# Performance work log

Measured on AMD Instinct MI355X. Metric: run time of the kernel, lower is better.

## Reference

```python
import jax, jax.numpy as jnp
import numpy as np

B, L, EMB = 256, 200, 128   # batch, low_capsule_num, emb_dim
HCN, HD = 1000, 64          # h_caps_num = poi_num//20, h_caps_dim
POI = 20000
EPS = 1e-8


def squash(s):
    # standard capsule squash along last dim
    sq = jnp.sum(s * s, axis=-1, keepdims=True)
    return (sq / (1.0 + sq)) * s / jnp.sqrt(sq + EPS)


def setup_inputs() -> dict:
    key = jax.random.key(0)
    ks = jax.random.split(key, 5)
    return {
        "u": jax.random.normal(ks[0], (B, L, EMB), jnp.float32),
        "l_map_h": jax.random.normal(ks[1], (EMB, HD), jnp.float32),
        "route_weights": jax.random.normal(ks[2], (1, HCN, L), jnp.float32),
        "w_dim": jax.random.normal(ks[3], (1, HD), jnp.float32) * 0.1,
        "b_dim": jnp.zeros((1,), jnp.float32),
        "w_part": jax.random.normal(ks[4], (POI, HCN), jnp.float32) * 0.03,
        "b_part": jnp.zeros((POI,), jnp.float32),
        "rn": 3,
    }


def reference(u, l_map_h, route_weights, w_dim, b_dim, w_part, b_part, rn):
    # u: [B, L, EMB] -> u_map: [B, L, HD]
    u_map = jnp.matmul(u, l_map_h)
    b = route_weights  # [1, HCN, L], non-trainable in the original
    v = None
    for _ in range(rn):
        c = jax.nn.softmax(b, axis=-1)            # [1, HCN, L]
        s = jnp.matmul(c, u_map)                  # broadcast -> [B, HCN, HD]
        v = squash(s)                             # [B, HCN, HD]
        # torch: sum over batch of v @ u_map^T, keepdim; .data update (detached)
        u_v = jnp.einsum('bhd,bld->hl', v, u_map)[None]  # [1, HCN, L]
        b = b + jax.lax.stop_gradient(u_v)
    # dim_linear_1 (Linear(HD,1)) then squeeze; dropout is identity (eval)
    h = jnp.squeeze(jnp.matmul(v, w_dim.T) + b_dim, axis=-1)  # [B, HCN]
    out = jnp.matmul(h, w_part.T) + b_part                     # [B, POI]
    return out
```

## Files before the change

### kernel.cpp

```cpp
#include <hip/hip_runtime.h>

#define B_    256
#define L_    200
#define EMB_  128
#define HD_   64
#define HCN_  1000
#define POI_  20000
#define EPS_  1e-8f
#define CP    224
#define UNR   208
#define NSLAB 64
#define SROW  1024
#define SPL   208

#define CSC   16384.0f
#define USC   256.0f
#define VSC   1024.0f
#define AUSC  1024.0f
#define LUSC  1024.0f
#define SV_DESC (1.0f / (CSC * USC))
#define UV_DESC (1.0f / (VSC * USC))
#define UM_DESC (1.0f / (AUSC * LUSC))

typedef _Float16 half8 __attribute__((ext_vector_type(8)));
typedef __bf16  bf16x8 __attribute__((ext_vector_type(8)));
typedef float   f32x4  __attribute__((ext_vector_type(4)));
typedef float   f32x16 __attribute__((ext_vector_type(16)));

__device__ __forceinline__ unsigned short f2bf(float f) {
  union { float f; unsigned int u; } v; v.f = f;
  unsigned int r = (v.u + 0x7FFFu + ((v.u >> 16) & 1u)) >> 16;
  return (unsigned short)r;
}
__device__ __forceinline__ void split2h(float x, _Float16& s1, _Float16& s2) {
  s1 = (_Float16)x;
  s2 = (_Float16)(x - (float)s1);
}

#define THREEPASS(acc, A1f, A2f, B1f, B2f)                                 \
  acc = __builtin_amdgcn_mfma_f32_16x16x32_f16(A2f, B1f, acc, 0, 0, 0);    \
  acc = __builtin_amdgcn_mfma_f32_16x16x32_f16(A1f, B2f, acc, 0, 0, 0);    \
  acc = __builtin_amdgcn_mfma_f32_16x16x32_f16(A1f, B1f, acc, 0, 0, 0);

__global__ __launch_bounds__(256, 2) void k_umap(const float* __restrict__ u,
                                                 const float* __restrict__ lmap,
                                                 float* __restrict__ umap) {
  __shared__ __align__(16) _Float16 lmT[2][64][136];
  __shared__ __align__(16) _Float16 uA[4][2][16][136];
  const int tid = threadIdx.x;
  for (int i = tid; i < 128 * 64; i += 256) {
    int k = i >> 6, d = i & 63;
    _Float16 s1, s2;
    split2h(lmap[i] * LUSC, s1, s2);
    lmT[0][d][k] = s1;
    lmT[1][d][k] = s2;
  }
  __syncthreads();

  const int wave = tid >> 6, lane = tid & 63;
  const int l15 = lane & 15, oc = lane >> 4;

  for (int t = 0; t < 4; ++t) {
    const int row0 = (blockIdx.x * 16 + wave * 4 + t) * 16;
    {
      const int r_ = lane >> 2, seg = lane & 3;
      const float* src = u + (size_t)(row0 + r_) * EMB_ + seg * 32;
#pragma unroll
      for (int j = 0; j < 8; ++j) {
        float4 v = *(const float4*)(src + j * 4);
        _Float16 t1[4], t2[4];
        split2h(v.x * AUSC, t1[0], t2[0]);
        split2h(v.y * AUSC, t1[1], t2[1]);
        split2h(v.z * AUSC, t1[2], t2[2]);
        split2h(v.w * AUSC, t1[3], t2[3]);
        const int kb = seg * 32 + j * 4;
        *(uint2*)&uA[wave][0][r_][kb] = *(uint2*)t1;
        *(uint2*)&uA[wave][1][r_][kb] = *(uint2*)t2;
      }
    }
    f32x4 acc[4] = {};
#pragma unroll
    for (int ck = 0; ck < 4; ++ck) {
      const half8 a1 = *(const half8*)&uA[wave][0][l15][ck * 32 + oc * 8];
      const half8 a2 = *(const half8*)&uA[wave][1][l15][ck * 32 + oc * 8];
#pragma unroll
      for (int nt = 0; nt < 4; ++nt) {
        const half8 b1 = *(const half8*)&lmT[0][nt * 16 + l15][ck * 32 + oc * 8];
        const half8 b2 = *(const half8*)&lmT[1][nt * 16 + l15][ck * 32 + oc * 8];
        THREEPASS(acc[nt], a1, a2, b1, b2);
      }
    }
#pragma unroll
    for (int nt = 0; nt < 4; ++nt)
#pragma unroll
      for (int r = 0; r < 4; ++r)
        umap[(size_t)(row0 + oc * 4 + r) * HD_ + nt * 16 + l15] = acc[nt][r] * UM_DESC;
  }
}

__global__ __launch_bounds__(256) void k_prep2(const float* __restrict__ umap,
    _Float16* __restrict__ un1, _Float16* __restrict__ un2,
    _Float16* __restrict__ ut1, _Float16* __restrict__ ut2) {
  __shared__ __align__(16) float us[CP][68];
  const int b = blockIdx.x;
  const float* ub = umap + (size_t)b * L_ * HD_;
  for (int i = threadIdx.x; i < CP * HD_; i += 256) {
    int l = i >> 6, d = i & 63;
    us[l][d] = (l < L_) ? ub[l * HD_ + d] * USC : 0.f;
  }
  __syncthreads();
  for (int s = threadIdx.x; s < UNR * 8; s += 256) {
    int row = s >> 3, oct = s & 7;
    _Float16 t1[8], t2[8];
#pragma unroll
    for (int j = 0; j < 8; ++j) split2h(us[row][oct * 8 + j], t1[j], t2[j]);
    size_t dst = ((size_t)b * UNR + row) * HD_ + oct * 8;
    *(uint4*)&un1[dst] = *(uint4*)t1;
    *(uint4*)&un2[dst] = *(uint4*)t2;
  }
  for (int s = threadIdx.x; s < HD_ * 28; s += 256) {
    int d = s / 28, lo8 = s % 28;
    _Float16 t1[8], t2[8];
#pragma unroll
    for (int j = 0; j < 8; ++j) split2h(us[lo8 * 8 + j][d], t1[j], t2[j]);
    size_t dst = ((size_t)b * HD_ + d) * CP + lo8 * 8;
    *(uint4*)&ut1[dst] = *(uint4*)t1;
    *(uint4*)&ut2[dst] = *(uint4*)t2;
  }
}

template<int SUM>
__global__ __launch_bounds__(256) void k_softmax2(float* __restrict__ bl,
    const float* __restrict__ part,
    _Float16* __restrict__ c1, _Float16* __restrict__ c2) {
  const int wave = threadIdx.x >> 6, lane = threadIdx.x & 63;
  const int row = blockIdx.x * 4 + wave;
  const size_t rb = (size_t)row * CP;
  if (row >= HCN_) {
    c1[rb + lane] = (_Float16)0.f;       c2[rb + lane] = (_Float16)0.f;
    c1[rb + lane + 64] = (_Float16)0.f;  c2[rb + lane + 64] = (_Float16)0.f;
    c1[rb + lane + 128] = (_Float16)0.f; c2[rb + lane + 128] = (_Float16)0.f;
    if (lane < 32) { c1[rb + 192 + lane] = (_Float16)0.f; c2[rb + 192 + lane] = (_Float16)0.f; }
    return;
  }
  float* br = bl + (size_t)row * L_;
  float x0 = br[lane];
  float x1 = br[lane + 64];
  float x2 = br[lane + 128];
  float x3 = (lane < 8) ? br[lane + 192] : -3.0e38f;
  if (SUM) {
#pragma unroll 8
    for (int s = 0; s < NSLAB; ++s) {
      const float* p = part + ((size_t)s * SROW + row) * SPL;
      x0 += __builtin_nontemporal_load(p + lane);
      x1 += __builtin_nontemporal_load(p + lane + 64);
      x2 += __builtin_nontemporal_load(p + lane + 128);
      if (lane < 8) x3 += __builtin_nontemporal_load(p + lane + 192);
    }
    br[lane] = x0; br[lane + 64] = x1; br[lane + 128] = x2;
    if (lane < 8) br[lane + 192] = x3;
  }
  float m = fmaxf(fmaxf(x0, x1), fmaxf(x2, x3));
#pragma unroll
  for (int off = 32; off; off >>= 1) m = fmaxf(m, __shfl_xor(m, off));
  float e0 = expf(x0 - m), e1 = expf(x1 - m), e2 = expf(x2 - m);
  float e3 = (lane < 8) ? expf(x3 - m) : 0.f;
  float ssum = e0 + e1 + e2 + e3;
#pragma unroll
  for (int off = 32; off; off >>= 1) ssum += __shfl_xor(ssum, off);
  float inv = CSC / ssum;
  _Float16 s1, s2;
  split2h(e0 * inv, s1, s2); c1[rb + lane] = s1;       c2[rb + lane] = s2;
  split2h(e1 * inv, s1, s2); c1[rb + lane + 64] = s1;  c2[rb + lane + 64] = s2;
  split2h(e2 * inv, s1, s2); c1[rb + lane + 128] = s1; c2[rb + lane + 128] = s2;
  if (lane < 8) {
    split2h(e3 * inv, s1, s2); c1[rb + 192 + lane] = s1; c2[rb + 192 + lane] = s2;
  } else if (lane < 32) {
    c1[rb + 192 + lane] = (_Float16)0.f; c2[rb + 192 + lane] = (_Float16)0.f;
  }
}

template<int UV, int HOUT>
__global__ __launch_bounds__(256, 4) void k_iter(
    const _Float16* __restrict__ c1p, const _Float16* __restrict__ c2p,
    const _Float16* __restrict__ un1, const _Float16* __restrict__ un2,
    const _Float16* __restrict__ ut1, const _Float16* __restrict__ ut2,
    const float* __restrict__ wdim, const float* __restrict__ bdim,
    float* __restrict__ part, unsigned short* __restrict__ hb) {
  __shared__ __align__(16) _Float16 smem[10240];
  __shared__ __align__(16) _Float16 v_sm[UV ? (2 * 64 * 72) : 2];
  typedef _Float16 (*UTarr)[2][64][40];
  typedef _Float16 (*UNarr)[112][40];
  typedef _Float16 (*VSarr)[64][72];
  UTarr UT = reinterpret_cast<UTarr>(smem);
  UNarr UN = reinterpret_cast<UNarr>(smem);
  VSarr VS = reinterpret_cast<VSarr>(v_sm);

  const int id = blockIdx.x;
  const int xcd = id & 7;
  const int ht  = (id >> 3) & 15;
  const int bgH = id >> 7;
  const int bg  = xcd + (bgH << 3);
  const int h0 = ht * 64;
  const int b0 = bg * 4;
  const int tid = threadIdx.x;
  const int wave = tid >> 6, lane = tid & 63;
  const int l15 = lane & 15, oc = lane >> 4;
  const int rowA = h0 + wave * 16 + l15;
  const int rowC = h0 + wave * 16 + oc * 4;

#define STAGE_UT(cck, bf) {                                                    \
    const int d_ = tid >> 2, q_ = tid & 3;                                     \
    const size_t so_ = ((size_t)b * HD_ + d_) * CP + (cck) * 32 + q_ * 8;      \
    *(uint4*)&UT[bf][0][d_][q_ * 8] = *(const uint4*)&ut1[so_];                \
    *(uint4*)&UT[bf][1][d_][q_ * 8] = *(const uint4*)&ut2[so_];                \
  }

#define STAGE_UN2(half_, g_, nrows_) {                                        \
    _Pragma("unroll")                                                          \
    for (int j_ = 0; j_ < 2; ++j_) {                                           \
      int t_ = tid + 256 * j_;                                                 \
      if (t_ < (nrows_) * 4) {                                                 \
        int row_ = t_ >> 2, q_ = t_ & 3;                                       \
        const size_t so_ = ((size_t)b * UNR + (g_) * 112 + row_) * HD_         \
                           + (half_) * 32 + q_ * 8;                            \
        *(uint4*)&UN[0][row_][q_ * 8] = *(const uint4*)&un1[so_];              \
        *(uint4*)&UN[1][row_][q_ * 8] = *(const uint4*)&un2[so_];              \
      } } }

  half8 a_f[7][2];
#pragma unroll
  for (int ck = 0; ck < 7; ++ck) {
    const size_t off = (size_t)rowA * CP + ck * 32 + oc * 8;
    a_f[ck][0] = *(const half8*)&c1p[off];
    a_f[ck][1] = *(const half8*)&c2p[off];
  }

  f32x4 acc_uv[13];
  if (UV) {
#pragma unroll
    for (int nt = 0; nt < 13; ++nt) acc_uv[nt] = (f32x4){0.f, 0.f, 0.f, 0.f};
  }
  float wd[4] = {0.f, 0.f, 0.f, 0.f};
  float bd = 0.f;
  if (HOUT) {
#pragma unroll
    for (int nt = 0; nt < 4; ++nt) wd[nt] = wdim[nt * 16 + l15];
    bd = bdim[0];
  }

  for (int bi = 0; bi < 4; ++bi) {
    const int b = b0 + bi;
    f32x4 acc_s[4];
#pragma unroll
    for (int nt = 0; nt < 4; ++nt) acc_s[nt] = (f32x4){0.f, 0.f, 0.f, 0.f};
    STAGE_UT(0, 0);
    __syncthreads();
#pragma unroll
    for (int ck = 0; ck < 7; ++ck) {
      if (ck < 6) STAGE_UT(ck + 1, (ck + 1) & 1);
      const int cb = ck & 1;
#pragma unroll
      for (int nt = 0; nt < 4; ++nt) {
        const half8 b1 = *(const half8*)&UT[cb][0][nt * 16 + l15][oc * 8];
        const half8 b2 = *(const half8*)&UT[cb][1][nt * 16 + l15][oc * 8];
        THREEPASS(acc_s[nt], a_f[ck][0], a_f[ck][1], b1, b2);
      }
      __syncthreads();
    }
    float xdesc[4][4];
#pragma unroll
    for (int nt = 0; nt < 4; ++nt)
#pragma unroll
      for (int r = 0; r < 4; ++r) xdesc[nt][r] = acc_s[nt][r] * SV_DESC;
    float gg[4], hq[4];
#pragma unroll
    for (int r = 0; r < 4; ++r) {
      float sq = 0.f, hpp = 0.f;
#pragma unroll
      for (int nt = 0; nt < 4; ++nt) {
        float x = xdesc[nt][r];
        sq += x * x;
        if (HOUT) hpp += x * wd[nt];
      }
#pragma unroll
      for (int off = 8; off; off >>= 1) {
        sq += __shfl_xor(sq, off);
        if (HOUT) hpp += __shfl_xor(hpp, off);
      }
      gg[r] = sq / ((1.f + sq) * sqrtf(sq + EPS_));
      if (HOUT) hq[r] = gg[r] * hpp + bd;
    }
    if (HOUT && l15 == 0) {
      ushort4 hv4;
      if (rowC < HCN_) {
        hv4.x = f2bf(hq[0]); hv4.y = f2bf(hq[1]);
        hv4.z = f2bf(hq[2]); hv4.w = f2bf(hq[3]);
      } else {
        hv4.x = hv4.y = hv4.z = hv4.w = 0;
      }
      *(ushort4*)&hb[(size_t)b * 1024 + rowC] = hv4;
    }
    if (UV) {
#pragma unroll
      for (int nt = 0; nt < 4; ++nt)
#pragma unroll
        for (int r = 0; r < 4; ++r) {
          _Float16 s1, s2;
          split2h(VSC * gg[r] * xdesc[nt][r], s1, s2);
          const int vr = wave * 16 + oc * 4 + r, vc = nt * 16 + l15;
          VS[0][vr][vc] = s1; VS[1][vr][vc] = s2;
        }
      __syncthreads();
#pragma unroll
      for (int half = 0; half < 2; ++half) {
        const int vo = half * 32 + oc * 8;
        const half8 av1 = *(const half8*)&VS[0][wave * 16 + l15][vo];
        const half8 av2 = *(const half8*)&VS[1][wave * 16 + l15][vo];
#pragma unroll
        for (int g = 0; g < 2; ++g) {
          STAGE_UN2(half, g, (g ? 96 : 112));
          __syncthreads();
          if (g == 0) {
#pragma unroll
            for (int nt = 0; nt < 7; ++nt) {
              const half8 b1 = *(const half8*)&UN[0][nt * 16 + l15][oc * 8];
              const half8 b2 = *(const half8*)&UN[1][nt * 16 + l15][oc * 8];
              THREEPASS(acc_uv[nt], av1, av2, b1, b2);
            }
          } else {
#pragma unroll
            for (int nt = 7; nt < 13; ++nt) {
              const half8 b1 = *(const half8*)&UN[0][(nt - 7) * 16 + l15][oc * 8];
              const half8 b2 = *(const half8*)&UN[1][(nt - 7) * 16 + l15][oc * 8];
              THREEPASS(acc_uv[nt], av1, av2, b1, b2);
            }
          }
          __syncthreads();
        }
      }
    }
  }
  if (UV) {
    float* pp = part + (size_t)bg * SROW * SPL;
#pragma unroll
    for (int r = 0; r < 4; ++r) {
      float* rowp = pp + (size_t)(rowC + r) * SPL + l15;
#pragma unroll
      for (int nt = 0; nt < 13; ++nt)
        __builtin_nontemporal_store(acc_uv[nt][r] * UV_DESC, rowp + nt * 16);
    }
  }
#undef STAGE_UT
#undef STAGE_UN2
}

#define KPAD 1024
#define LPITCH 72
__global__ __launch_bounds__(512) void k_out_mfma(const unsigned short* __restrict__ hb,
                                                  const float* __restrict__ wpart,
                                                  const float* __restrict__ bpart,
                                                  float* __restrict__ out) {
  __shared__ __align__(16) unsigned short w_lds[128 * LPITCH];
  __shared__ __align__(16) unsigned short h_lds[128 * LPITCH];
  const int p0 = blockIdx.x * 128;
  const int b0 = blockIdx.y * 128;
  const int t = threadIdx.x;
  const int wave = t >> 6, lane = t & 63;
  const int nt = wave & 3, mh = wave >> 2;
  const int l31 = lane & 31, lhi = lane >> 5;

  f32x16 acc0 = {};
  f32x16 acc1 = {};

  const int wrow = t >> 2;
  const int wq0  = (t & 3) * 4;
  int prow = p0 + wrow; if (prow > POI_ - 1) prow = POI_ - 1;
  const float* wrp = wpart + (size_t)prow * HCN_;

  for (int ch = 0; ch < 16; ++ch) {
    const int k0 = ch * 64;
    __syncthreads();
#pragma unroll
    for (int qq = 0; qq < 4; ++qq) {
      const int q = wq0 + qq;
      float4 wv;
      if (k0 + q * 4 + 3 < HCN_) {
        wv = *(const float4*)(wrp + k0 + q * 4);
      } else {
        float x0 = (k0 + q * 4 + 0 < HCN_) ? wrp[k0 + q * 4 + 0] : 0.f;
        float x1 = (k0 + q * 4 + 1 < HCN_) ? wrp[k0 + q * 4 + 1] : 0.f;
        float x2 = (k0 + q * 4 + 2 < HCN_) ? wrp[k0 + q * 4 + 2] : 0.f;
        float x3 = (k0 + q * 4 + 3 < HCN_) ? wrp[k0 + q * 4 + 3] : 0.f;
        wv = make_float4(x0, x1, x2, x3);
      }
      ushort4 bv;
      bv.x = f2bf(wv.x); bv.y = f2bf(wv.y); bv.z = f2bf(wv.z); bv.w = f2bf(wv.w);
      *(ushort4*)&w_lds[wrow * LPITCH + q * 4] = bv;
    }
#pragma unroll
    for (int n = 0; n < 2; ++n) {
      const int u = t + n * 512;
      const int hrow = u >> 3, hc = u & 7;
      const uint4 hv = *(const uint4*)(hb + (size_t)(b0 + hrow) * KPAD + k0 + hc * 8);
      *(uint4*)&h_lds[hrow * LPITCH + hc * 8] = hv;
    }
    __syncthreads();
#pragma unroll
    for (int ks = 0; ks < 4; ++ks) {
      const int kc = ks * 16 + lhi * 8;
      bf16x8 bfr = *(const bf16x8*)&w_lds[(nt * 32 + l31) * LPITCH + kc];
      bf16x8 a0  = *(const bf16x8*)&h_lds[(mh * 64 + 0 * 32 + l31) * LPITCH + kc];
      bf16x8 a1  = *(const bf16x8*)&h_lds[(mh * 64 + 1 * 32 + l31) * LPITCH + kc];
      acc0 = __builtin_amdgcn_mfma_f32_32x32x16_bf16(a0, bfr, acc0, 0, 0, 0);
      acc1 = __builtin_amdgcn_mfma_f32_32x32x16_bf16(a1, bfr, acc1, 0, 0, 0);
    }
  }

  const int p = p0 + nt * 32 + l31;
  const bool pok = (p < POI_);
  const float bp = pok ? bpart[p] : 0.f;
#pragma unroll
  for (int m = 0; m < 2; ++m) {
    const f32x16& a = m ? acc1 : acc0;
#pragma unroll
    for (int r = 0; r < 16; ++r) {
      const int brow = b0 + mh * 64 + m * 32 + (r & 3) + 8 * (r >> 2) + 4 * lhi;
      if (pok) out[(size_t)brow * POI_ + p] = a[r] + bp;
    }
  }
}

extern "C" void kernel_launch(void* const* d_in, const int* in_sizes, int n_in,
                              void* d_out, int out_size, void* d_ws, size_t ws_size,
                              hipStream_t stream) {
  const float* u     = (const float*)d_in[0];
  const float* lmap  = (const float*)d_in[1];
  const float* rw    = (const float*)d_in[2];
  const float* wdim  = (const float*)d_in[3];
  const float* bdim  = (const float*)d_in[4];
  const float* wpart = (const float*)d_in[5];
  const float* bpart = (const float*)d_in[6];
  float* out = (float*)d_out;

  char* W = (char*)d_ws;
  float* bl        = (float*)W;      W += 802816;
  _Float16* c1     = (_Float16*)W;   W += 458752;
  _Float16* c2     = (_Float16*)W;   W += 458752;
  _Float16* un1    = (_Float16*)W;   W += 6815744;
  _Float16* un2    = (_Float16*)W;   W += 6815744;
  _Float16* ut1    = (_Float16*)W;   W += 7340032;
  _Float16* ut2    = (_Float16*)W;   W += 7340032;
  unsigned short* h_bf16 = (unsigned short*)W; W += 524288;
  float* part      = (float*)W;      W += (size_t)NSLAB * SROW * SPL * 4;
  float* umap      = part;

  hipMemcpyAsync(bl, rw, (size_t)HCN_ * L_ * sizeof(float),
                 hipMemcpyDeviceToDevice, stream);
  k_umap<<<200, 256, 0, stream>>>(u, lmap, umap);
  k_prep2<<<256, 256, 0, stream>>>(umap, un1, un2, ut1, ut2);

  k_softmax2<0><<<256, 256, 0, stream>>>(bl, part, c1, c2);
  k_iter<1, 0><<<1024, 256, 0, stream>>>(c1, c2, un1, un2, ut1, ut2,
                                         wdim, bdim, part, h_bf16);
  k_softmax2<1><<<256, 256, 0, stream>>>(bl, part, c1, c2);
  k_iter<1, 0><<<1024, 256, 0, stream>>>(c1, c2, un1, un2, ut1, ut2,
                                         wdim, bdim, part, h_bf16);
  k_softmax2<1><<<256, 256, 0, stream>>>(bl, part, c1, c2);
  k_iter<0, 1><<<1024, 256, 0, stream>>>(c1, c2, un1, un2, ut1, ut2,
                                         wdim, bdim, part, h_bf16);

  k_out_mfma<<<dim3(157, 2), 512, 0, stream>>>(h_bf16, wpart, bpart, out);
}
```

Before: 380.5 us.

## Double k_iter block to 512 threads with 8 batches and split work across wave halves

k_iter now runs 512-thread blocks. Each block handles 8 batches instead of 4, which halves the number of partial-sum slabs and the grid size. The two wave halves split the HD dimension for the s computation and combine squared norms through shared memory. They also split the L columns for the u_v accumulation, and the full 208-row u_map slice is staged at once instead of in two chunks. This aims to cut partial-slab write and reduce traffic and barrier count, at the cost of extra LDS use, a cross-wave reduction sync, and possibly lower occupancy.

```diff
diff --git a/kernel.cpp b/kernel.cpp
--- a/kernel.cpp
+++ b/kernel.cpp
@@ -9,7 +9,7 @@
 #define EPS_  1e-8f
 #define CP    224
 #define UNR   208
-#define NSLAB 64
+#define NSLAB 32
 #define SROW  1024
 #define SPL   208
 
@@ -181,16 +181,18 @@
 }
 
 template<int UV, int HOUT>
-__global__ __launch_bounds__(256, 4) void k_iter(
+__global__ __launch_bounds__(512, 4) void k_iter(
     const _Float16* __restrict__ c1p, const _Float16* __restrict__ c2p,
     const _Float16* __restrict__ un1, const _Float16* __restrict__ un2,
     const _Float16* __restrict__ ut1, const _Float16* __restrict__ ut2,
     const float* __restrict__ wdim, const float* __restrict__ bdim,
     float* __restrict__ part, unsigned short* __restrict__ hb) {
-  __shared__ __align__(16) _Float16 smem[10240];
+  __shared__ __align__(16) _Float16 smem[16640];
   __shared__ __align__(16) _Float16 v_sm[UV ? (2 * 64 * 72) : 2];
+  __shared__ __align__(16) float sqx[2][64];
+  __shared__ __align__(16) float hpx[2][64];
   typedef _Float16 (*UTarr)[2][64][40];
-  typedef _Float16 (*UNarr)[112][40];
+  typedef _Float16 (*UNarr)[208][40];
   typedef _Float16 (*VSarr)[64][72];
   UTarr UT = reinterpret_cast<UTarr>(smem);
   UNarr UN = reinterpret_cast<UNarr>(smem);
@@ -202,28 +204,29 @@
   const int bgH = id >> 7;
   const int bg  = xcd + (bgH << 3);
   const int h0 = ht * 64;
-  const int b0 = bg * 4;
+  const int b0 = bg * 8;
   const int tid = threadIdx.x;
   const int wave = tid >> 6, lane = tid & 63;
+  const int hsub = wave & 3, ksub = wave >> 2;
   const int l15 = lane & 15, oc = lane >> 4;
-  const int rowA = h0 + wave * 16 + l15;
-  const int rowC = h0 + wave * 16 + oc * 4;
+  const int rowA = h0 + hsub * 16 + l15;
+  const int rowL = hsub * 16 + oc * 4;
+  const int rowC = h0 + rowL;
 
 #define STAGE_UT(cck, bf) {                                                    \
-    const int d_ = tid >> 2, q_ = tid & 3;                                     \
-    const size_t so_ = ((size_t)b * HD_ + d_) * CP + (cck) * 32 + q_ * 8;      \
-    *(uint4*)&UT[bf][0][d_][q_ * 8] = *(const uint4*)&ut1[so_];                \
-    *(uint4*)&UT[bf][1][d_][q_ * 8] = *(const uint4*)&ut2[so_];                \
-  }
-
-#define STAGE_UN2(half_, g_, nrows_) {                                        \
+    const int sp_ = tid >> 8, d_ = (tid >> 2) & 63, q_ = tid & 3;              \
+    const _Float16* s_ = sp_ ? ut2 : ut1;                                      \
+    *(uint4*)&UT[bf][sp_][d_][q_ * 8] =                                        \
+      *(const uint4*)&s_[((size_t)b * HD_ + d_) * CP + (cck) * 32 + q_ * 8];   \
+  }
+
+#define STAGE_UN(half_) {                                                      \
     _Pragma("unroll")                                                          \
     for (int j_ = 0; j_ < 2; ++j_) {                                           \
-      int t_ = tid + 256 * j_;                                                 \
-      if (t_ < (nrows_) * 4) {                                                 \
+      int t_ = tid + 512 * j_;                                                 \
+      if (t_ < 832) {                                                          \
         int row_ = t_ >> 2, q_ = t_ & 3;                                       \
-        const size_t so_ = ((size_t)b * UNR + (g_) * 112 + row_) * HD_         \
-                           + (half_) * 32 + q_ * 8;                            \
+        const size_t so_ = ((size_t)b * UNR + row_) * HD_ + (half_) * 32 + q_ * 8; \
         *(uint4*)&UN[0][row_][q_ * 8] = *(const uint4*)&un1[so_];              \
         *(uint4*)&UN[1][row_][q_ * 8] = *(const uint4*)&un2[so_];              \
       } } }
@@ -236,24 +239,24 @@
     a_f[ck][1] = *(const half8*)&c2p[off];
   }
 
-  f32x4 acc_uv[13];
+  f32x4 acc_uv[7];
   if (UV) {
 #pragma unroll
-    for (int nt = 0; nt < 13; ++nt) acc_uv[nt] = (f32x4){0.f, 0.f, 0.f, 0.f};
-  }
-  float wd[4] = {0.f, 0.f, 0.f, 0.f};
+    for (int nt = 0; nt < 7; ++nt) acc_uv[nt] = (f32x4){0.f, 0.f, 0.f, 0.f};
+  }
+  float wd[2] = {0.f, 0.f};
   float bd = 0.f;
   if (HOUT) {
 #pragma unroll
-    for (int nt = 0; nt < 4; ++nt) wd[nt] = wdim[nt * 16 + l15];
+    for (int j = 0; j < 2; ++j) wd[j] = wdim[(ksub * 2 + j) * 16 + l15];
     bd = bdim[0];
   }
 
-  for (int bi = 0; bi < 4; ++bi) {
+  for (int bi = 0; bi < 8; ++bi) {
     const int b = b0 + bi;
-    f32x4 acc_s[4];
-#pragma unroll
-    for (int nt = 0; nt < 4; ++nt) acc_s[nt] = (f32x4){0.f, 0.f, 0.f, 0.f};
+    f32x4 acc_s[2];
+#pragma unroll
+    for (int j = 0; j < 2; ++j) acc_s[j] = (f32x4){0.f, 0.f, 0.f, 0.f};
     STAGE_UT(0, 0);
     __syncthreads();
 #pragma unroll
@@ -261,37 +264,49 @@
       if (ck < 6) STAGE_UT(ck + 1, (ck + 1) & 1);
       const int cb = ck & 1;
 #pragma unroll
-      for (int nt = 0; nt < 4; ++nt) {
-        const half8 b1 = *(const half8*)&UT[cb][0][nt * 16 + l15][oc * 8];
-        const half8 b2 = *(const half8*)&UT[cb][1][nt * 16 + l15][oc * 8];
-        THREEPASS(acc_s[nt], a_f[ck][0], a_f[ck][1], b1, b2);
+      for (int j = 0; j < 2; ++j) {
+        const half8 b1 = *(const half8*)&UT[cb][0][(ksub * 2 + j) * 16 + l15][oc * 8];
+        const half8 b2 = *(const half8*)&UT[cb][1][(ksub * 2 + j) * 16 + l15][oc * 8];
+        THREEPASS(acc_s[j], a_f[ck][0], a_f[ck][1], b1, b2);
       }
       __syncthreads();
     }
-    float xdesc[4][4];
-#pragma unroll
-    for (int nt = 0; nt < 4; ++nt)
-#pragma unroll
-      for (int r = 0; r < 4; ++r) xdesc[nt][r] = acc_s[nt][r] * SV_DESC;
-    float gg[4], hq[4];
+    float xd[2][4];
+#pragma unroll
+    for (int j = 0; j < 2; ++j)
+#pragma unroll
+      for (int r = 0; r < 4; ++r) xd[j][r] = acc_s[j][r] * SV_DESC;
+    float sqp[4], hpp[4];
 #pragma unroll
     for (int r = 0; r < 4; ++r) {
-      float sq = 0.f, hpp = 0.f;
-#pragma unroll
-      for (int nt = 0; nt < 4; ++nt) {
-        float x = xdesc[nt][r];
-        sq += x * x;
-        if (HOUT) hpp += x * wd[nt];
-      }
+      float sq = xd[0][r] * xd[0][r] + xd[1][r] * xd[1][r];
+      float hp = 0.f;
+      if (HOUT) hp = xd[0][r] * wd[0] + xd[1][r] * wd[1];
 #pragma unroll
       for (int off = 8; off; off >>= 1) {
         sq += __shfl_xor(sq, off);
-        if (HOUT) hpp += __shfl_xor(hpp, off);
-      }
-      gg[r] = sq / ((1.f + sq) * sqrtf(sq + EPS_));
-      if (HOUT) hq[r] = gg[r] * hpp + bd;
-    }
-    if (HOUT && l15 == 0) {
+        if (HOUT) hp += __shfl_xor(hp, off);
+      }
+      sqp[r] = sq;
+      hpp[r] = hp;
+    }
+    if (l15 == 0) {
+#pragma unroll
+      for (int r = 0; r < 4; ++r) {
+        sqx[ksub][rowL + r] = sqp[r];
+        if (HOUT) hpx[ksub][rowL + r] = hpp[r];
+      }
+    }
+    if (UV) STAGE_UN(0);
+    __syncthreads();
+    float gg[4], hq[4];
+#pragma unroll
+    for (int r = 0; r < 4; ++r) {
+      float st = sqp[r] + sqx[1 - ksub][rowL + r];
+      gg[r] = st / ((1.f + st) * sqrtf(st + EPS_));
+      if (HOUT) hq[r] = gg[r] * (hpp[r] + hpx[1 - ksub][rowL + r]) + bd;
+    }
+    if (HOUT && ksub == 0 && l15 == 0) {
       ushort4 hv4;
       if (rowC < HCN_) {
         hv4.x = f2bf(hq[0]); hv4.y = f2bf(hq[1]);
@@ -303,56 +318,50 @@
     }
     if (UV) {
 #pragma unroll
-      for (int nt = 0; nt < 4; ++nt)
+      for (int j = 0; j < 2; ++j)
 #pragma unroll
         for (int r = 0; r < 4; ++r) {
           _Float16 s1, s2;
-          split2h(VSC * gg[r] * xdesc[nt][r], s1, s2);
-          const int vr = wave * 16 + oc * 4 + r, vc = nt * 16 + l15;
+          split2h(VSC * gg[r] * xd[j][r], s1, s2);
+          const int vr = rowL + r, vc = (ksub * 2 + j) * 16 + l15;
           VS[0][vr][vc] = s1; VS[1][vr][vc] = s2;
         }
       __syncthreads();
 #pragma unroll
       for (int half = 0; half < 2; ++half) {
-        const int vo = half * 32 + oc * 8;
-        const half8 av1 = *(const half8*)&VS[0][wave * 16 + l15][vo];
-        const half8 av2 = *(const half8*)&VS[1][wave * 16 + l15][vo];
-#pragma unroll
-        for (int g = 0; g < 2; ++g) {
-          STAGE_UN2(half, g, (g ? 96 : 112));
+        if (half == 1) {
           __syncthreads();
-          if (g == 0) {
-#pragma unroll
-            for (int nt = 0; nt < 7; ++nt) {
-              const half8 b1 = *(const half8*)&UN[0][nt * 16 + l15][oc * 8];
-              const half8 b2 = *(const half8*)&UN[1][nt * 16 + l15][oc * 8];
-              THREEPASS(acc_uv[nt], av1, av2, b1, b2);
-            }
-          } else {
-#pragma unroll
-            for (int nt = 7; nt < 13; ++nt) {
-              const half8 b1 = *(const half8*)&UN[0][(nt - 7) * 16 + l15][oc * 8];
-              const half8 b2 = *(const half8*)&UN[1][(nt - 7) * 16 + l15][oc * 8];
-              THREEPASS(acc_uv[nt], av1, av2, b1, b2);
-            }
-          }
+          STAGE_UN(1);
           __syncthreads();
         }
-      }
+        const int vo = half * 32 + oc * 8;
+        const half8 av1 = *(const half8*)&VS[0][hsub * 16 + l15][vo];
+        const half8 av2 = *(const half8*)&VS[1][hsub * 16 + l15][vo];
+#pragma unroll
+        for (int nt = 0; nt < 7; ++nt) {
+          int urow = (nt + ksub * 7) * 16 + l15;
+          if (urow > 207) urow = 207;
+          const half8 b1 = *(const half8*)&UN[0][urow][oc * 8];
+          const half8 b2 = *(const half8*)&UN[1][urow][oc * 8];
+          THREEPASS(acc_uv[nt], av1, av2, b1, b2);
+        }
+      }
+      __syncthreads();
     }
   }
   if (UV) {
     float* pp = part + (size_t)bg * SROW * SPL;
 #pragma unroll
     for (int r = 0; r < 4; ++r) {
-      float* rowp = pp + (size_t)(rowC + r) * SPL + l15;
-#pragma unroll
-      for (int nt = 0; nt < 13; ++nt)
-        __builtin_nontemporal_store(acc_uv[nt][r] * UV_DESC, rowp + nt * 16);
+      float* rowp = pp + (size_t)(rowC + r) * SPL + ksub * 112 + l15;
+#pragma unroll
+      for (int nt = 0; nt < 7; ++nt)
+        if (nt + ksub * 7 <= 12)
+          __builtin_nontemporal_store(acc_uv[nt][r] * UV_DESC, rowp + nt * 16);
     }
   }
 #undef STAGE_UT
-#undef STAGE_UN2
+#undef STAGE_UN
 }
 
 #define KPAD 1024
@@ -461,14 +470,14 @@
   k_prep2<<<256, 256, 0, stream>>>(umap, un1, un2, ut1, ut2);
 
   k_softmax2<0><<<256, 256, 0, stream>>>(bl, part, c1, c2);
-  k_iter<1, 0><<<1024, 256, 0, stream>>>(c1, c2, un1, un2, ut1, ut2,
-                                         wdim, bdim, part, h_bf16);
+  k_iter<1, 0><<<512, 512, 0, stream>>>(c1, c2, un1, un2, ut1, ut2,
+                                        wdim, bdim, part, h_bf16);
   k_softmax2<1><<<256, 256, 0, stream>>>(bl, part, c1, c2);
-  k_iter<1, 0><<<1024, 256, 0, stream>>>(c1, c2, un1, un2, ut1, ut2,
-                                         wdim, bdim, part, h_bf16);
+  k_iter<1, 0><<<512, 512, 0, stream>>>(c1, c2, un1, un2, ut1, ut2,
+                                        wdim, bdim, part, h_bf16);
   k_softmax2<1><<<256, 256, 0, stream>>>(bl, part, c1, c2);
-  k_iter<0, 1><<<1024, 256, 0, stream>>>(c1, c2, un1, un2, ut1, ut2,
-                                         wdim, bdim, part, h_bf16);
+  k_iter<0, 1><<<512, 512, 0, stream>>>(c1, c2, un1, un2, ut1, ut2,
+                                        wdim, bdim, part, h_bf16);
 
   k_out_mfma<<<dim3(157, 2), 512, 0, stream>>>(h_bf16, wpart, bpart, out);
 }
```

Measured after the change: 366.0 us. 3.8% less time.

## Double k_iter block tile to 128 capsules and widen LDS staging chunks

Applied to the files above, without the earlier changes.

Each k_iter block now handles 128 high capsules with 8 waves (512 threads) instead of 64 with 4 waves. This halves the grid and the number of times each u_map slab is staged per batch row. The UT staging chunks grow from 32 to 64 columns, and the UN stage loads all 208 rows at once, which cuts the number of syncthreads rounds. In exchange the kernel uses more LDS per block and fewer blocks, so occupancy and latency hiding may drop.

```diff
diff --git a/kernel.cpp b/kernel.cpp
--- a/kernel.cpp
+++ b/kernel.cpp
@@ -181,49 +181,61 @@
 }
 
 template<int UV, int HOUT>
-__global__ __launch_bounds__(256, 4) void k_iter(
+__global__ __launch_bounds__(512, 2) void k_iter(
     const _Float16* __restrict__ c1p, const _Float16* __restrict__ c2p,
     const _Float16* __restrict__ un1, const _Float16* __restrict__ un2,
     const _Float16* __restrict__ ut1, const _Float16* __restrict__ ut2,
     const float* __restrict__ wdim, const float* __restrict__ bdim,
     float* __restrict__ part, unsigned short* __restrict__ hb) {
-  __shared__ __align__(16) _Float16 smem[10240];
-  __shared__ __align__(16) _Float16 v_sm[UV ? (2 * 64 * 72) : 2];
-  typedef _Float16 (*UTarr)[2][64][40];
-  typedef _Float16 (*UNarr)[112][40];
-  typedef _Float16 (*VSarr)[64][72];
+  __shared__ __align__(16) _Float16 smem[18432];
+  __shared__ __align__(16) _Float16 v_sm[UV ? (2 * 128 * 72) : 2];
+  typedef _Float16 (*UTarr)[2][64][72];
+  typedef _Float16 (*UNarr)[208][40];
+  typedef _Float16 (*VSarr)[128][72];
   UTarr UT = reinterpret_cast<UTarr>(smem);
   UNarr UN = reinterpret_cast<UNarr>(smem);
   VSarr VS = reinterpret_cast<VSarr>(v_sm);
 
   const int id = blockIdx.x;
   const int xcd = id & 7;
-  const int ht  = (id >> 3) & 15;
-  const int bgH = id >> 7;
+  const int ht  = (id >> 3) & 7;
+  const int bgH = id >> 6;
   const int bg  = xcd + (bgH << 3);
-  const int h0 = ht * 64;
+  const int h0 = ht * 128;
   const int b0 = bg * 4;
   const int tid = threadIdx.x;
   const int wave = tid >> 6, lane = tid & 63;
   const int l15 = lane & 15, oc = lane >> 4;
   const int rowA = h0 + wave * 16 + l15;
-  const int rowC = h0 + wave * 16 + oc * 4;
-
-#define STAGE_UT(cck, bf) {                                                    \
-    const int d_ = tid >> 2, q_ = tid & 3;                                     \
-    const size_t so_ = ((size_t)b * HD_ + d_) * CP + (cck) * 32 + q_ * 8;      \
-    *(uint4*)&UT[bf][0][d_][q_ * 8] = *(const uint4*)&ut1[so_];                \
-    *(uint4*)&UT[bf][1][d_][q_ * 8] = *(const uint4*)&ut2[so_];                \
-  }
-
-#define STAGE_UN2(half_, g_, nrows_) {                                        \
+  const int rowL = wave * 16 + oc * 4;
+  const int rowC = h0 + rowL;
+
+#define STAGE_UT64(cck, bf) {                                                  \
     _Pragma("unroll")                                                          \
     for (int j_ = 0; j_ < 2; ++j_) {                                           \
-      int t_ = tid + 256 * j_;                                                 \
-      if (t_ < (nrows_) * 4) {                                                 \
+      int s_ = tid + 512 * j_;                                                 \
+      int sp_ = s_ >> 9, rem_ = s_ & 511;                                      \
+      int d_ = rem_ >> 3, q_ = rem_ & 7;                                       \
+      const _Float16* src_ = sp_ ? ut2 : ut1;                                  \
+      *(uint4*)&UT[bf][sp_][d_][q_ * 8] =                                      \
+        *(const uint4*)&src_[((size_t)b * HD_ + d_) * CP + (cck) * 64 + q_ * 8]; \
+    } }
+
+#define STAGE_UT32(bf) {                                                       \
+    int sp_ = tid >> 8, rem_ = tid & 255;                                      \
+    int d_ = rem_ >> 2, q_ = rem_ & 3;                                         \
+    const _Float16* src_ = sp_ ? ut2 : ut1;                                    \
+    *(uint4*)&UT[bf][sp_][d_][q_ * 8] =                                        \
+      *(const uint4*)&src_[((size_t)b * HD_ + d_) * CP + 192 + q_ * 8];        \
+  }
+
+#define STAGE_UN(half_) {                                                      \
+    _Pragma("unroll")                                                          \
+    for (int j_ = 0; j_ < 2; ++j_) {                                           \
+      int t_ = tid + 512 * j_;                                                 \
+      if (t_ < 832) {                                                          \
         int row_ = t_ >> 2, q_ = t_ & 3;                                       \
-        const size_t so_ = ((size_t)b * UNR + (g_) * 112 + row_) * HD_         \
-                           + (half_) * 32 + q_ * 8;                            \
+        const size_t so_ = ((size_t)b * UNR + row_) * HD_ + (half_) * 32 + q_ * 8; \
         *(uint4*)&UN[0][row_][q_ * 8] = *(const uint4*)&un1[so_];              \
         *(uint4*)&UN[1][row_][q_ * 8] = *(const uint4*)&un2[so_];              \
       } } }
@@ -254,19 +266,29 @@
     f32x4 acc_s[4];
 #pragma unroll
     for (int nt = 0; nt < 4; ++nt) acc_s[nt] = (f32x4){0.f, 0.f, 0.f, 0.f};
-    STAGE_UT(0, 0);
+    STAGE_UT64(0, 0);
     __syncthreads();
 #pragma unroll
-    for (int ck = 0; ck < 7; ++ck) {
-      if (ck < 6) STAGE_UT(ck + 1, (ck + 1) & 1);
+    for (int ck = 0; ck < 3; ++ck) {
+      if (ck < 2) STAGE_UT64(ck + 1, (ck + 1) & 1)
+      else        STAGE_UT32(1)
       const int cb = ck & 1;
 #pragma unroll
       for (int nt = 0; nt < 4; ++nt) {
-        const half8 b1 = *(const half8*)&UT[cb][0][nt * 16 + l15][oc * 8];
-        const half8 b2 = *(const half8*)&UT[cb][1][nt * 16 + l15][oc * 8];
-        THREEPASS(acc_s[nt], a_f[ck][0], a_f[ck][1], b1, b2);
-      }
-      __syncthreads();
+#pragma unroll
+        for (int sub = 0; sub < 2; ++sub) {
+          const half8 b1 = *(const half8*)&UT[cb][0][nt * 16 + l15][sub * 32 + oc * 8];
+          const half8 b2 = *(const half8*)&UT[cb][1][nt * 16 + l15][sub * 32 + oc * 8];
+          THREEPASS(acc_s[nt], a_f[ck * 2 + sub][0], a_f[ck * 2 + sub][1], b1, b2);
+        }
+      }
+      __syncthreads();
+    }
+#pragma unroll
+    for (int nt = 0; nt < 4; ++nt) {
+      const half8 b1 = *(const half8*)&UT[1][0][nt * 16 + l15][oc * 8];
+      const half8 b2 = *(const half8*)&UT[1][1][nt * 16 + l15][oc * 8];
+      THREEPASS(acc_s[nt], a_f[6][0], a_f[6][1], b1, b2);
     }
     float xdesc[4][4];
 #pragma unroll
@@ -308,37 +330,38 @@
         for (int r = 0; r < 4; ++r) {
           _Float16 s1, s2;
           split2h(VSC * gg[r] * xdesc[nt][r], s1, s2);
-          const int vr = wave * 16 + oc * 4 + r, vc = nt * 16 + l15;
+          const int vr = rowL + r, vc = nt * 16 + l15;
           VS[0][vr][vc] = s1; VS[1][vr][vc] = s2;
         }
       __syncthreads();
-#pragma unroll
-      for (int half = 0; half < 2; ++half) {
-        const int vo = half * 32 + oc * 8;
-        const half8 av1 = *(const half8*)&VS[0][wave * 16 + l15][vo];
-        const half8 av2 = *(const half8*)&VS[1][wave * 16 + l15][vo];
-#pragma unroll
-        for (int g = 0; g < 2; ++g) {
-          STAGE_UN2(half, g, (g ? 96 : 112));
-          __syncthreads();
-          if (g == 0) {
-#pragma unroll
-            for (int nt = 0; nt < 7; ++nt) {
-              const half8 b1 = *(const half8*)&UN[0][nt * 16 + l15][oc * 8];
-              const half8 b2 = *(const half8*)&UN[1][nt * 16 + l15][oc * 8];
-              THREEPASS(acc_uv[nt], av1, av2, b1, b2);
-            }
-          } else {
-#pragma unroll
-            for (int nt = 7; nt < 13; ++nt) {
-              const half8 b1 = *(const half8*)&UN[0][(nt - 7) * 16 + l15][oc * 8];
-              const half8 b2 = *(const half8*)&UN[1][(nt - 7) * 16 + l15][oc * 8];
-              THREEPASS(acc_uv[nt], av1, av2, b1, b2);
-            }
-          }
-          __syncthreads();
+      STAGE_UN(0);
+      __syncthreads();
+      {
+        const half8 av1 = *(const half8*)&VS[0][wave * 16 + l15][oc * 8];
+        const half8 av2 = *(const half8*)&VS[1][wave * 16 + l15][oc * 8];
+#pragma unroll
+        for (int nt = 0; nt < 13; ++nt) {
+          const half8 b1 = *(const half8*)&UN[0][nt * 16 + l15][oc * 8];
+          const half8 b2 = *(const half8*)&UN[1][nt * 16 + l15][oc * 8];
+          THREEPASS(acc_uv[nt], av1, av2, b1, b2);
         }
       }
+      __syncthreads();
+      STAGE_UN(1);
+      __syncthreads();
+      {
+        const half8 av1 = *(const half8*)&VS[0][wave * 16 + l15][32 + oc * 8];
+        const half8 av2 = *(const half8*)&VS[1][wave * 16 + l15][32 + oc * 8];
+#pragma unroll
+        for (int nt = 0; nt < 13; ++nt) {
+          const half8 b1 = *(const half8*)&UN[0][nt * 16 + l15][oc * 8];
+          const half8 b2 = *(const half8*)&UN[1][nt * 16 + l15][oc * 8];
+          THREEPASS(acc_uv[nt], av1, av2, b1, b2);
+        }
+      }
+      __syncthreads();
+    } else {
+      __syncthreads();
     }
   }
   if (UV) {
@@ -351,8 +374,9 @@
         __builtin_nontemporal_store(acc_uv[nt][r] * UV_DESC, rowp + nt * 16);
     }
   }
-#undef STAGE_UT
-#undef STAGE_UN2
+#undef STAGE_UT64
+#undef STAGE_UT32
+#undef STAGE_UN
 }
 
 #define KPAD 1024
@@ -461,14 +485,14 @@
   k_prep2<<<256, 256, 0, stream>>>(umap, un1, un2, ut1, ut2);
 
   k_softmax2<0><<<256, 256, 0, stream>>>(bl, part, c1, c2);
-  k_iter<1, 0><<<1024, 256, 0, stream>>>(c1, c2, un1, un2, ut1, ut2,
-                                         wdim, bdim, part, h_bf16);
+  k_iter<1, 0><<<512, 512, 0, stream>>>(c1, c2, un1, un2, ut1, ut2,
+                                        wdim, bdim, part, h_bf16);
   k_softmax2<1><<<256, 256, 0, stream>>>(bl, part, c1, c2);
-  k_iter<1, 0><<<1024, 256, 0, stream>>>(c1, c2, un1, un2, ut1, ut2,
-                                         wdim, bdim, part, h_bf16);
+  k_iter<1, 0><<<512, 512, 0, stream>>>(c1, c2, un1, un2, ut1, ut2,
+                                        wdim, bdim, part, h_bf16);
   k_softmax2<1><<<256, 256, 0, stream>>>(bl, part, c1, c2);
-  k_iter<0, 1><<<1024, 256, 0, stream>>>(c1, c2, un1, un2, ut1, ut2,
-                                         wdim, bdim, part, h_bf16);
+  k_iter<0, 1><<<512, 512, 0, stream>>>(c1, c2, un1, un2, ut1, ut2,
+                                        wdim, bdim, part, h_bf16);
 
   k_out_mfma<<<dim3(157, 2), 512, 0, stream>>>(h_bf16, wpart, bpart, out);
 }
```

Measured after the change: 344.7 us. -9.4%, faster.
